# Kernel optimization log

Hardware: AMD Instinct MI355X
Metric: run time of the kernel (lower is better)

## Reference

```python
import jax, jax.numpy as jnp
import numpy as np

D_MODEL = 768
H = 12
D_K = D_MODEL // H


def setup_inputs() -> dict:
    key = jax.random.key(0)
    ks = jax.random.split(key, 12)
    B, S = 2, 2048
    scale = 1.0 / np.sqrt(D_MODEL)
    q = jax.random.normal(ks[0], (B, S, D_MODEL), jnp.float32)
    k = jax.random.normal(ks[1], (B, S, D_MODEL), jnp.float32)
    v = jax.random.normal(ks[2], (B, S, D_MODEL), jnp.float32)
    mask = jnp.tril(jnp.ones((S, S), jnp.int32))[None, None]  # causal [1,1,S,S]
    wq = jax.random.normal(ks[3], (D_MODEL, D_MODEL), jnp.float32) * scale
    wk = jax.random.normal(ks[4], (D_MODEL, D_MODEL), jnp.float32) * scale
    wv = jax.random.normal(ks[5], (D_MODEL, D_MODEL), jnp.float32) * scale
    wo = jax.random.normal(ks[6], (D_MODEL, D_MODEL), jnp.float32) * scale
    bq = jax.random.normal(ks[7], (D_MODEL,), jnp.float32) * 0.02
    bk = jax.random.normal(ks[8], (D_MODEL,), jnp.float32) * 0.02
    bv = jax.random.normal(ks[9], (D_MODEL,), jnp.float32) * 0.02
    bo = jax.random.normal(ks[10], (D_MODEL,), jnp.float32) * 0.02
    return {"q": q, "k": k, "v": v, "mask": mask,
            "wq": wq, "bq": bq, "wk": wk, "bk": bk,
            "wv": wv, "bv": bv, "wo": wo, "bo": bo}


def reference(q, k, v, mask, wq, bq, wk, bk, wv, bv, wo, bo):
    B, S, _ = q.shape
    # projections (torch Linear: x @ W.T + b)
    qh = (q @ wq.T + bq).reshape(B, S, H, D_K).transpose(0, 2, 1, 3)  # [B,H,S,Dk]
    kh = (k @ wk.T + bk).reshape(B, S, H, D_K).transpose(0, 2, 1, 3)
    vh = (v @ wv.T + bv).reshape(B, S, H, D_K).transpose(0, 2, 1, 3)
    scores = jnp.einsum('bhqd,bhkd->bhqk', qh, kh) / np.sqrt(D_K)
    scores = jnp.where(mask == 0, -jnp.inf, scores)
    attn = jax.nn.softmax(scores, axis=-1)  # dropout p=0.0 (eval) -> identity
    x = jnp.einsum('bhqk,bhkd->bhqd', attn, vh)
    x = x.transpose(0, 2, 1, 3).reshape(B, S, D_MODEL)
    return x @ wo.T + bo
```

## Files before the change

kernel.cpp:

```cpp
#include <hip/hip_runtime.h>
#include <hip/hip_bf16.h>

#define DM 768
#define NH 12
#define DK 64
#define SEQ 2048
#define NB 2
#define M_ (NB*SEQ)
#define XN 3145728
#define WN 589824

typedef __bf16 bf16;
typedef bf16 bf16x2 __attribute__((ext_vector_type(2)));
typedef bf16 bf16x4 __attribute__((ext_vector_type(4)));
typedef bf16 bf16x8 __attribute__((ext_vector_type(8)));
typedef float f32x4 __attribute__((ext_vector_type(4)));

__device__ __forceinline__ f32x4 mfma16(bf16x8 a, bf16x8 b, f32x4 c) {
    return __builtin_amdgcn_mfma_f32_16x16x32_bf16(a, b, c, 0, 0, 0);
}

__device__ __forceinline__ void gload_lds16(const bf16* g, bf16* l) {
    __builtin_amdgcn_global_load_lds(
        (const __attribute__((address_space(1))) void*)g,
        (__attribute__((address_space(3))) void*)l, 16, 0, 0);
}

__global__ __launch_bounds__(256) void convert_kernel(
    const float* __restrict__ q, const float* __restrict__ k, const float* __restrict__ v,
    const float* __restrict__ wq, const float* __restrict__ wk, const float* __restrict__ wv,
    const float* __restrict__ wo, bf16* __restrict__ Xb, bf16* __restrict__ Wb)
{
    long long e = ((long long)blockIdx.x * 256 + threadIdx.x) * 8;
    const float* src; bf16* dst;
    if (e < 3LL * XN) {
        int z = (int)(e / XN);
        src = (z == 0 ? q : z == 1 ? k : v) + (e - (long long)z * XN);
        dst = Xb + e;
    } else {
        long long e2 = e - 3LL * XN;
        int z = (int)(e2 / WN);
        src = (z == 0 ? wq : z == 1 ? wk : z == 2 ? wv : wo) + (e2 - (long long)z * WN);
        dst = Wb + e2;
    }
    f32x4 a = *(const f32x4*)src;
    f32x4 b = *(const f32x4*)(src + 4);
    bf16x8 o;
#pragma unroll
    for (int j = 0; j < 4; ++j) { o[j] = (bf16)a[j]; o[j + 4] = (bf16)b[j]; }
    *(bf16x8*)dst = o;
}

__global__ __launch_bounds__(256) void qkv_gemm_kernel(
    const bf16* __restrict__ Xb, const bf16* __restrict__ Wb,
    const float* __restrict__ bq, const float* __restrict__ bk, const float* __restrict__ bv,
    bf16* __restrict__ Qh, bf16* __restrict__ Kh, bf16* __restrict__ Vt)
{
    __shared__ bf16 lds[12288];
    int z = blockIdx.z;
    const bf16* Ab = Xb + (size_t)z * XN;
    const bf16* Wz = Wb + (size_t)z * WN;
    const float* Bi = (z == 0) ? bq : (z == 1) ? bk : bv;

    int t = threadIdx.x;
    int lane = t & 63, w = t >> 6;
    int g = lane >> 4, c = lane & 15;
    int wm = (w >> 1) * 64, wn = (w & 1) * 32;
    int m0 = blockIdx.x * 128, n0 = blockIdx.y * 64;

    f32x4 acc[4][2] = {};

    const bf16* Agp[4];
#pragma unroll
    for (int r = 0; r < 4; ++r) {
        int e = r * 2048 + t * 8;
        int kk = e >> 12, mm = (e & 4095) >> 5, k8 = e & 31;
        Agp[r] = Ab + (size_t)(m0 + mm) * DM + kk * 32 + k8;
    }
    const bf16* Bgp[2];
#pragma unroll
    for (int r = 0; r < 2; ++r) {
        int e = r * 2048 + t * 8;
        int kk = e >> 11, nn = (e & 2047) >> 5, k8 = e & 31;
        Bgp[r] = Wz + (size_t)(n0 + nn) * DM + kk * 32 + k8;
    }

    for (int kt = 0; kt < 12; ++kt) {
#pragma unroll
        for (int r = 0; r < 4; ++r)
            gload_lds16(Agp[r] + kt * 64, &lds[r * 2048 + t * 8]);
#pragma unroll
        for (int r = 0; r < 2; ++r)
            gload_lds16(Bgp[r] + kt * 64, &lds[8192 + r * 2048 + t * 8]);
        __syncthreads();
        bf16x8 af[4][2], bfr[2][2];
#pragma unroll
        for (int kk = 0; kk < 2; ++kk) {
#pragma unroll
            for (int mi = 0; mi < 4; ++mi)
                af[mi][kk] = *(const bf16x8*)&lds[kk * 4096 + (wm + mi * 16 + c) * 32 + g * 8];
#pragma unroll
            for (int ni = 0; ni < 2; ++ni)
                bfr[ni][kk] = *(const bf16x8*)&lds[8192 + kk * 2048 + (wn + ni * 16 + c) * 32 + g * 8];
        }
#pragma unroll
        for (int mi = 0; mi < 4; ++mi)
#pragma unroll
            for (int ni = 0; ni < 2; ++ni) {
                acc[mi][ni] = mfma16(af[mi][0], bfr[ni][0], acc[mi][ni]);
                acc[mi][ni] = mfma16(af[mi][1], bfr[ni][1], acc[mi][ni]);
            }
        __syncthreads();
    }

    int b_ = m0 >> 11, sbase = m0 & (SEQ - 1);
    int h = blockIdx.y;
    if (z == 0) {
#pragma unroll
        for (int ni = 0; ni < 2; ++ni) {
            int nl = wn + ni * 16 + c;
            float bias = Bi[n0 + nl];
#pragma unroll
            for (int mi = 0; mi < 4; ++mi)
#pragma unroll
                for (int r = 0; r < 4; ++r) {
                    int s = sbase + wm + mi * 16 + g * 4 + r;
                    Qh[((size_t)(b_ * NH + h) * SEQ + s) * DK + nl] = (bf16)(acc[mi][ni][r] + bias);
                }
        }
    } else if (z == 1) {
#pragma unroll
        for (int ni = 0; ni < 2; ++ni) {
            int nl = wn + ni * 16 + c;
            float bias = Bi[n0 + nl];
            int chunk = nl >> 3, e = nl & 7;
#pragma unroll
            for (int mi = 0; mi < 4; ++mi)
#pragma unroll
                for (int r = 0; r < 4; ++r) {
                    int s = sbase + wm + mi * 16 + g * 4 + r;
                    int pos = ((chunk ^ (s & 7)) << 3) + e;
                    Kh[((size_t)(b_ * NH + h) * SEQ + s) * DK + pos] = (bf16)(acc[mi][ni][r] + bias);
                }
        }
    } else {
#pragma unroll
        for (int ni = 0; ni < 2; ++ni) {
            int nl = wn + ni * 16 + c;
            float bias = Bi[n0 + nl];
#pragma unroll
            for (int mi = 0; mi < 4; ++mi) {
                bf16x4 pk;
#pragma unroll
                for (int r = 0; r < 4; ++r) pk[r] = (bf16)(acc[mi][ni][r] + bias);
                int sb = wm + mi * 16;
                int grp64 = sb >> 6, grp = (sb >> 5) & 1, bb = (sb >> 4) & 1;
                int chi = 4 * grp + g;
                int col = grp64 * 64 + ((chi ^ (nl & 7)) << 3) + 4 * bb;
                *(bf16x4*)&lds[nl * 136 + col] = pk;
            }
        }
        __syncthreads();
        int dk = t >> 2, sc = (t & 3) * 32;
        bf16* vdst = Vt + ((size_t)(b_ * NH + h) * DK + dk) * SEQ + sbase + sc;
#pragma unroll
        for (int j = 0; j < 4; ++j)
            *(bf16x8*)(vdst + j * 8) = *(const bf16x8*)&lds[dk * 136 + sc + j * 8];
    }
}

__global__ __launch_bounds__(256) void o_gemm_kernel(
    const bf16* __restrict__ Xo, const bf16* __restrict__ Wo,
    const float* __restrict__ bo, float* __restrict__ out)
{
    __shared__ bf16 lds[12288];
    int t = threadIdx.x;
    int lane = t & 63, w = t >> 6;
    int g = lane >> 4, c = lane & 15;
    int wm = (w >> 1) * 64, wn = (w & 1) * 32;
    int m0 = blockIdx.x * 128, n0 = blockIdx.y * 64;

    f32x4 acc[4][2] = {};

    const bf16* Agp[4];
#pragma unroll
    for (int r = 0; r < 4; ++r) {
        int e = r * 2048 + t * 8;
        int kk = e >> 12, mm = (e & 4095) >> 5, k8 = e & 31;
        Agp[r] = Xo + (size_t)(m0 + mm) * DM + kk * 32 + k8;
    }
    const bf16* Bgp[2];
#pragma unroll
    for (int r = 0; r < 2; ++r) {
        int e = r * 2048 + t * 8;
        int kk = e >> 11, nn = (e & 2047) >> 5, k8 = e & 31;
        Bgp[r] = Wo + (size_t)(n0 + nn) * DM + kk * 32 + k8;
    }

    for (int kt = 0; kt < 12; ++kt) {
#pragma unroll
        for (int r = 0; r < 4; ++r)
            gload_lds16(Agp[r] + kt * 64, &lds[r * 2048 + t * 8]);
#pragma unroll
        for (int r = 0; r < 2; ++r)
            gload_lds16(Bgp[r] + kt * 64, &lds[8192 + r * 2048 + t * 8]);
        __syncthreads();
        bf16x8 af[4][2], bfr[2][2];
#pragma unroll
        for (int kk = 0; kk < 2; ++kk) {
#pragma unroll
            for (int mi = 0; mi < 4; ++mi)
                af[mi][kk] = *(const bf16x8*)&lds[kk * 4096 + (wm + mi * 16 + c) * 32 + g * 8];
#pragma unroll
            for (int ni = 0; ni < 2; ++ni)
                bfr[ni][kk] = *(const bf16x8*)&lds[8192 + kk * 2048 + (wn + ni * 16 + c) * 32 + g * 8];
        }
#pragma unroll
        for (int mi = 0; mi < 4; ++mi)
#pragma unroll
            for (int ni = 0; ni < 2; ++ni) {
                acc[mi][ni] = mfma16(af[mi][0], bfr[ni][0], acc[mi][ni]);
                acc[mi][ni] = mfma16(af[mi][1], bfr[ni][1], acc[mi][ni]);
            }
        __syncthreads();
    }

#pragma unroll
    for (int ni = 0; ni < 2; ++ni) {
        int n = n0 + wn + ni * 16 + c;
        float bias = bo[n];
#pragma unroll
        for (int mi = 0; mi < 4; ++mi)
#pragma unroll
            for (int r = 0; r < 4; ++r)
                out[(size_t)(m0 + wm + mi * 16 + g * 4 + r) * DM + n] = acc[mi][ni][r] + bias;
    }
}

__global__ __launch_bounds__(256) void attn_part_kernel(
    const bf16* __restrict__ Qh, const bf16* __restrict__ Kh, const bf16* __restrict__ Vt,
    bf16* __restrict__ Po, float* __restrict__ Pml)
{
    __shared__ bf16 kt_lds[2][4096];
    __shared__ bf16 vt_lds[2][4096];

    int blk = blockIdx.x;
    int bh = blk % (NB * NH);
    int idx = blk / (NB * NH);
    int J = 31 - (idx >> 1);
    int s = idx & 1;
    int t = threadIdx.x;
    int w = t >> 6, lane = t & 63;
    int g = lane >> 4, c = lane & 15;
    int sw = c & 7;
    const bf16* Qb = Qh + (size_t)bh * SEQ * DK;
    const bf16* Kb = Kh + (size_t)bh * SEQ * DK;
    const bf16* Vb = Vt + (size_t)bh * DK * SEQ;

    const float SCL = 0.125f * 1.4426950408889634f;

    int qa = J * 64 + w * 16;
    int myq = qa + c;
    int nkt = J + 1;
    int tiles0 = (nkt + 1) >> 1;
    int kt_begin = s ? tiles0 : 0;
    int kt_end   = s ? nkt : tiles0;

    float l_st = 0.f;
    f32x4 o[4] = {};

    if (kt_begin < kt_end) {
        bf16x8 qf0 = *(const bf16x8*)(Qb + (size_t)(qa + c) * DK + g * 8);
        bf16x8 qf1 = *(const bf16x8*)(Qb + (size_t)(qa + c) * DK + 32 + g * 8);

        auto stage = [&](int kt, int buf) {
            int kb = kt * 64;
            const bf16* kg = Kb + (size_t)kb * DK + t * 8;
#pragma unroll
            for (int i = 0; i < 2; ++i)
                gload_lds16(kg + i * 2048, &kt_lds[buf][i * 2048 + t * 8]);
            int dvr = t >> 3, colc = (t & 7) * 8;
            const bf16* vg = Vb + (size_t)dvr * SEQ + kb + colc;
#pragma unroll
            for (int i = 0; i < 2; ++i)
                gload_lds16(vg + (size_t)(32 * i) * SEQ, &vt_lds[buf][i * 2048 + t * 8]);
        };

        stage(kt_begin, kt_begin & 1);
        for (int kt = kt_begin; kt < kt_end; ++kt) {
            __syncthreads();
            if (kt + 1 < kt_end) stage(kt + 1, (kt + 1) & 1);
            int kb = kt * 64;
            int buf = kt & 1;
            bf16x8 kf[4][2];
#pragma unroll
            for (int i = 0; i < 4; ++i) {
                kf[i][0] = *(const bf16x8*)&kt_lds[buf][(16 * i + c) * 64 + ((g ^ sw) << 3)];
                kf[i][1] = *(const bf16x8*)&kt_lds[buf][(16 * i + c) * 64 + (((4 + g) ^ sw) << 3)];
            }
            bf16x8 vf[2][4];
#pragma unroll
            for (int grp = 0; grp < 2; ++grp)
#pragma unroll
                for (int t2 = 0; t2 < 4; ++t2)
                    vf[grp][t2] = *(const bf16x8*)&vt_lds[buf][(16 * t2 + c) * 64 + (((grp * 4 + g) ^ sw) << 3)];

            bool masked = (kb + 63 > qa);
            float p_[4][4];
#pragma unroll
            for (int i = 0; i < 4; ++i) {
                f32x4 a = {};
                a = mfma16(kf[i][0], qf0, a);
                a = mfma16(kf[i][1], qf1, a);
                if (masked) {
#pragma unroll
                    for (int r = 0; r < 4; ++r) {
                        int key = kb + i * 16 + g * 4 + r;
                        p_[i][r] = exp2f((key <= myq) ? a[r] * SCL : -INFINITY);
                    }
                } else {
#pragma unroll
                    for (int r = 0; r < 4; ++r) p_[i][r] = exp2f(a[r] * SCL);
                }
            }
            float s0_ = (p_[0][0] + p_[0][1]) + (p_[0][2] + p_[0][3]);
            float s1_ = (p_[1][0] + p_[1][1]) + (p_[1][2] + p_[1][3]);
            float s2_ = (p_[2][0] + p_[2][1]) + (p_[2][2] + p_[2][3]);
            float s3_ = (p_[3][0] + p_[3][1]) + (p_[3][2] + p_[3][3]);
            l_st += (s0_ + s1_) + (s2_ + s3_);
            bf16x8 pa0, pa1;
#pragma unroll
            for (int jj = 0; jj < 8; ++jj) {
                pa0[jj] = (bf16)p_[jj >> 2][jj & 3];
                pa1[jj] = (bf16)p_[2 + (jj >> 2)][jj & 3];
            }
#pragma unroll
            for (int t2 = 0; t2 < 4; ++t2) {
                o[t2] = mfma16(vf[0][t2], pa0, o[t2]);
                o[t2] = mfma16(vf[1][t2], pa1, o[t2]);
            }
        }
    }

    l_st += __shfl_xor(l_st, 16, 64);
    l_st += __shfl_xor(l_st, 32, 64);

    size_t base = ((((size_t)bh * 32 + J) * 2 + s) * 64 + w * 16 + c);
    if (g == 0) Pml[base] = l_st;
#pragma unroll
    for (int t2 = 0; t2 < 4; ++t2) {
        bf16x4 sa;
#pragma unroll
        for (int r = 0; r < 4; ++r) sa[r] = (bf16)o[t2][r];
        *(bf16x4*)&Po[base * 64 + t2 * 16 + g * 4] = sa;
    }
}

__global__ __launch_bounds__(256) void attn_merge_kernel(
    const bf16* __restrict__ Po, const float* __restrict__ Pml, bf16* __restrict__ Xo)
{
    int idx = blockIdx.x * 256 + threadIdx.x;
    int row = idx >> 2;
    int dq = (idx & 3) * 16;
    int bh = row >> 11;
    int rem = row & 2047;
    int J = rem >> 6, q = rem & 63;
    size_t b0 = (((size_t)bh * 32 + J) * 2 + 0) * 64 + q;
    size_t b1 = b0 + 64;
    float inv = 1.f / (Pml[b0] + Pml[b1]);
    int b_ = bh / NH, h = bh % NH;
    bf16* xrow = Xo + (size_t)(b_ * SEQ + J * 64 + q) * DM + h * DK + dq;
    const bf16* p0 = Po + b0 * 64 + dq;
    const bf16* p1 = Po + b1 * 64 + dq;
    bf16x8 v0a = *(const bf16x8*)p0, v0b = *(const bf16x8*)(p0 + 8);
    bf16x8 v1a = *(const bf16x8*)p1, v1b = *(const bf16x8*)(p1 + 8);
    bf16x8 oa, ob2;
#pragma unroll
    for (int j = 0; j < 8; ++j) {
        oa[j]  = (bf16)(((float)v0a[j] + (float)v1a[j]) * inv);
        ob2[j] = (bf16)(((float)v0b[j] + (float)v1b[j]) * inv);
    }
    *(bf16x8*)xrow = oa;
    *(bf16x8*)(xrow + 8) = ob2;
}

extern "C" void kernel_launch(void* const* d_in, const int* in_sizes, int n_in,
                              void* d_out, int out_size, void* d_ws, size_t ws_size,
                              hipStream_t stream) {
    const float* q  = (const float*)d_in[0];
    const float* k  = (const float*)d_in[1];
    const float* v  = (const float*)d_in[2];
    const float* wq = (const float*)d_in[4];
    const float* bq = (const float*)d_in[5];
    const float* wk = (const float*)d_in[6];
    const float* bk = (const float*)d_in[7];
    const float* wv = (const float*)d_in[8];
    const float* bv = (const float*)d_in[9];
    const float* wo = (const float*)d_in[10];
    const float* bo = (const float*)d_in[11];

    bf16* Xb = (bf16*)d_ws;
    bf16* Wb = Xb + 3 * (size_t)XN;
    bf16* Qh = Wb + 4 * (size_t)WN;
    bf16* Kh = Qh + (size_t)XN;
    bf16* Vt = Kh + (size_t)XN;
    bf16* Po = Vt + (size_t)XN;
    float* Pml = (float*)(Po + 6291456);
    bf16* Xo = Xb;
    float* out = (float*)d_out;

    dim3 blk(256);
    convert_kernel<<<dim3(5760), blk, 0, stream>>>(q, k, v, wq, wk, wv, wo, Xb, Wb);
    qkv_gemm_kernel<<<dim3(M_ / 128, DM / 64, 3), blk, 0, stream>>>(
        Xb, Wb, bq, bk, bv, Qh, Kh, Vt);
    attn_part_kernel<<<dim3(24 * 32 * 2), blk, 0, stream>>>(Qh, Kh, Vt, Po, Pml);
    attn_merge_kernel<<<dim3(768), blk, 0, stream>>>(Po, Pml, Xo);
    o_gemm_kernel<<<dim3(M_ / 128, DM / 64), blk, 0, stream>>>(Xo, Wb + 3 * (size_t)WN, bo, out);
}
```

Before: 185.9 us.

## Fuse attention partial merge into output projection GEMM A-operand load

Removes the separate merge kernel and instead combines the two split-KV partial outputs and normalizes them while loading the A tile of the output projection GEMM. A tiles are loaded into registers with one-step prefetch, merged and written to LDS, replacing async global-to-LDS loads. This saves a launch and the Xo round trip through memory, but every column block now re-reads both partials and recomputes the merge, and loses the direct-to-LDS load path.

```diff
diff --git a/kernel.cpp b/kernel.cpp
--- a/kernel.cpp
+++ b/kernel.cpp
@@ -170,8 +170,8 @@
 }
 
 __global__ __launch_bounds__(256) void o_gemm_kernel(
-    const bf16* __restrict__ Xo, const bf16* __restrict__ Wo,
-    const float* __restrict__ bo, float* __restrict__ out)
+    const bf16* __restrict__ Po, const float* __restrict__ Pml,
+    const bf16* __restrict__ Wo, const float* __restrict__ bo, float* __restrict__ out)
 {
     __shared__ bf16 lds[12288];
     int t = threadIdx.x;
@@ -182,12 +182,19 @@
 
     f32x4 acc[4][2] = {};
 
-    const bf16* Agp[4];
+    int Abase[4];
+    int Aoff[4];
+    int Al[4];
 #pragma unroll
     for (int r = 0; r < 4; ++r) {
         int e = r * 2048 + t * 8;
         int kk = e >> 12, mm = (e & 4095) >> 5, k8 = e & 31;
-        Agp[r] = Xo + (size_t)(m0 + mm) * DM + kk * 32 + k8;
+        int m = m0 + mm;
+        int b_ = m >> 11, s = m & (SEQ - 1);
+        int J = s >> 6, qq = s & 63;
+        Abase[r] = ((b_ * NH * 32 + J) * 2) * 64 + qq;
+        Aoff[r] = kk * 32 + k8;
+        Al[r] = e;
     }
     const bf16* Bgp[2];
 #pragma unroll
@@ -197,13 +204,36 @@
         Bgp[r] = Wo + (size_t)(n0 + nn) * DM + kk * 32 + k8;
     }
 
+    bf16x8 pa0[4], pa1[4];
+    float l0[4], l1[4];
+    auto loadA = [&](int kt) {
+#pragma unroll
+        for (int r = 0; r < 4; ++r) {
+            int base0 = Abase[r] + kt * 4096;
+            pa0[r] = *(const bf16x8*)&Po[(size_t)base0 * 64 + Aoff[r]];
+            pa1[r] = *(const bf16x8*)&Po[(size_t)(base0 + 64) * 64 + Aoff[r]];
+            l0[r] = Pml[base0];
+            l1[r] = Pml[base0 + 64];
+        }
+    };
+
+    loadA(0);
     for (int kt = 0; kt < 12; ++kt) {
-#pragma unroll
-        for (int r = 0; r < 4; ++r)
-            gload_lds16(Agp[r] + kt * 64, &lds[r * 2048 + t * 8]);
 #pragma unroll
         for (int r = 0; r < 2; ++r)
             gload_lds16(Bgp[r] + kt * 64, &lds[8192 + r * 2048 + t * 8]);
+        bf16x8 aw[4];
+#pragma unroll
+        for (int r = 0; r < 4; ++r) {
+            float inv = 1.f / (l0[r] + l1[r]);
+            bf16x8 v0 = pa0[r], v1 = pa1[r];
+#pragma unroll
+            for (int j = 0; j < 8; ++j)
+                aw[r][j] = (bf16)(((float)v0[j] + (float)v1[j]) * inv);
+        }
+        if (kt < 11) loadA(kt + 1);
+#pragma unroll
+        for (int r = 0; r < 4; ++r) *(bf16x8*)&lds[Al[r]] = aw[r];
         __syncthreads();
         bf16x8 af[4][2], bfr[2][2];
 #pragma unroll
@@ -354,34 +384,6 @@
         for (int r = 0; r < 4; ++r) sa[r] = (bf16)o[t2][r];
         *(bf16x4*)&Po[base * 64 + t2 * 16 + g * 4] = sa;
     }
-}
-
-__global__ __launch_bounds__(256) void attn_merge_kernel(
-    const bf16* __restrict__ Po, const float* __restrict__ Pml, bf16* __restrict__ Xo)
-{
-    int idx = blockIdx.x * 256 + threadIdx.x;
-    int row = idx >> 2;
-    int dq = (idx & 3) * 16;
-    int bh = row >> 11;
-    int rem = row & 2047;
-    int J = rem >> 6, q = rem & 63;
-    size_t b0 = (((size_t)bh * 32 + J) * 2 + 0) * 64 + q;
-    size_t b1 = b0 + 64;
-    float inv = 1.f / (Pml[b0] + Pml[b1]);
-    int b_ = bh / NH, h = bh % NH;
-    bf16* xrow = Xo + (size_t)(b_ * SEQ + J * 64 + q) * DM + h * DK + dq;
-    const bf16* p0 = Po + b0 * 64 + dq;
-    const bf16* p1 = Po + b1 * 64 + dq;
-    bf16x8 v0a = *(const bf16x8*)p0, v0b = *(const bf16x8*)(p0 + 8);
-    bf16x8 v1a = *(const bf16x8*)p1, v1b = *(const bf16x8*)(p1 + 8);
-    bf16x8 oa, ob2;
-#pragma unroll
-    for (int j = 0; j < 8; ++j) {
-        oa[j]  = (bf16)(((float)v0a[j] + (float)v1a[j]) * inv);
-        ob2[j] = (bf16)(((float)v0b[j] + (float)v1b[j]) * inv);
-    }
-    *(bf16x8*)xrow = oa;
-    *(bf16x8*)(xrow + 8) = ob2;
 }
 
 extern "C" void kernel_launch(void* const* d_in, const int* in_sizes, int n_in,
@@ -406,7 +408,6 @@
     bf16* Vt = Kh + (size_t)XN;
     bf16* Po = Vt + (size_t)XN;
     float* Pml = (float*)(Po + 6291456);
-    bf16* Xo = Xb;
     float* out = (float*)d_out;
 
     dim3 blk(256);
@@ -414,6 +415,5 @@
     qkv_gemm_kernel<<<dim3(M_ / 128, DM / 64, 3), blk, 0, stream>>>(
         Xb, Wb, bq, bk, bv, Qh, Kh, Vt);
     attn_part_kernel<<<dim3(24 * 32 * 2), blk, 0, stream>>>(Qh, Kh, Vt, Po, Pml);
-    attn_merge_kernel<<<dim3(768), blk, 0, stream>>>(Po, Pml, Xo);
-    o_gemm_kernel<<<dim3(M_ / 128, DM / 64), blk, 0, stream>>>(Xo, Wb + 3 * (size_t)WN, bo, out);
-}
+    o_gemm_kernel<<<dim3(M_ / 128, DM / 64), blk, 0, stream>>>(Po, Pml, Wb + 3 * (size_t)WN, bo, out);
+}
```

Result: no change. 188.6 us (+1.4%).
